# Kernel optimization log

Measured on AMD Instinct MI355X. Metric: run time of the kernel, lower is better.

Reference implementation:

```python
import jax, jax.numpy as jnp
import numpy as np

GRID_SIZE = 5
SPLINE_ORDER = 3
COEFF = GRID_SIZE + SPLINE_ORDER  # 8 spline coefficients per (out,in) pair
NUM_HEADS = 4
NUM_LAYERS = 4
DIM = 256
FF_DIM = 1024
VOCAB = 32000
EPS_EMB = 1e-12   # layernorm_eps from init
EPS_LN = 1e-5     # nn.LayerNorm default inside encoder layers


def make_grid(in_features):
    # uniform extended B-spline grid over [-1, 1], shape (in, grid_size + 2*order + 1)
    h = 2.0 / GRID_SIZE
    g = jnp.arange(-SPLINE_ORDER, GRID_SIZE + SPLINE_ORDER + 1, dtype=jnp.float32) * h - 1.0
    return jnp.broadcast_to(g, (in_features, g.shape[0]))


def b_splines(x, grid):
    # Cox-de Boor recursion. x: (..., in) -> (..., in, COEFF)
    xe = x[..., None]
    bases = ((xe >= grid[:, :-1]) & (xe < grid[:, 1:])).astype(x.dtype)
    for k in range(1, SPLINE_ORDER + 1):
        left = (xe - grid[:, : -(k + 1)]) / (grid[:, k:-1] - grid[:, : -(k + 1)])
        right = (grid[:, k + 1:] - xe) / (grid[:, k + 1:] - grid[:, 1:-k])
        bases = left * bases[..., :-1] + right * bases[..., 1:]
    return bases


def kan(x, base_w, spline_w):
    # efficient-kan KANLinear: silu base path + B-spline path
    grid = make_grid(x.shape[-1])
    base = jax.nn.silu(x) @ base_w.T
    spl = b_splines(x, grid)                      # (..., in, COEFF)
    return base + jnp.einsum('...ic,oic->...o', spl, spline_w)


def layer_norm(x, g=None, b=None, eps=EPS_LN):
    mu = jnp.mean(x, axis=-1, keepdims=True)
    var = jnp.mean((x - mu) ** 2, axis=-1, keepdims=True)
    y = (x - mu) * jax.lax.rsqrt(var + eps)
    return y * g + b if g is not None else y


def setup_inputs() -> dict:
    key = jax.random.key(0)
    ks = iter(jax.random.split(key, 64))

    def w(shape, s=0.02):
        return jax.random.normal(next(ks), shape, jnp.float32) * s

    inp = {
        'input_ids': jax.random.randint(next(ks), (2, 512), 0, VOCAB),
        'word_emb': w((VOCAB, DIM)),
        'tok_type_emb': w((2, DIM)),
        'pos_emb': w((512, DIM)),
        'emb_ln_g': jnp.ones((DIM,), jnp.float32),
        'emb_ln_b': jnp.zeros((DIM,), jnp.float32),
    }
    L = NUM_LAYERS
    for nm, (o, i) in [('q', (DIM, DIM)), ('k', (DIM, DIM)), ('v', (DIM, DIM)),
                       ('o', (DIM, DIM)), ('f1', (FF_DIM, DIM)), ('f2', (DIM, FF_DIM))]:
        inp[nm + '_base'] = w((L, o, i))
        inp[nm + '_spline'] = w((L, o, i, COEFF))
    inp['ln1_g'] = jnp.ones((L, DIM), jnp.float32)
    inp['ln1_b'] = jnp.zeros((L, DIM), jnp.float32)
    inp['ln2_g'] = jnp.ones((L, DIM), jnp.float32)
    inp['ln2_b'] = jnp.zeros((L, DIM), jnp.float32)
    inp['hk_base'] = w((DIM, DIM))
    inp['hk_spline'] = w((DIM, DIM, COEFF))
    inp['ho_base'] = w((VOCAB, DIM))
    inp['ho_spline'] = w((VOCAB, DIM, COEFF))
    return inp


def reference(input_ids, word_emb, tok_type_emb, pos_emb, emb_ln_g, emb_ln_b,
              q_base, q_spline, k_base, k_spline, v_base, v_spline,
              o_base, o_spline, f1_base, f1_spline, f2_base, f2_spline,
              ln1_g, ln1_b, ln2_g, ln2_b,
              hk_base, hk_spline, ho_base, ho_spline):
    B, S = input_ids.shape
    # Faithful to source: attention_mask defaults to ones_like(input_ids) and is
    # used to index BOTH token-type and positional embedding tables (row 1).
    x = word_emb[input_ids] + tok_type_emb[1] + pos_emb[1]
    x = layer_norm(x, emb_ln_g, emb_ln_b, eps=EPS_EMB)  # dropout = identity (deterministic)

    H, hd = NUM_HEADS, DIM // NUM_HEADS
    scale = hd ** -0.5
    for l in range(NUM_LAYERS):
        def split(t):
            return t.reshape(B, S, H, hd).transpose(0, 2, 1, 3)  # (B,H,S,hd)
        q = split(kan(x, q_base[l], q_spline[l]))
        k = split(kan(x, k_base[l], k_spline[l]))
        v = split(kan(x, v_base[l], v_spline[l]))
        attn = jax.nn.softmax(jnp.einsum('bhqd,bhkd->bhqk', q, k) * scale, axis=-1)
        ctx = jnp.einsum('bhqk,bhkd->bhqd', attn, v).transpose(0, 2, 1, 3).reshape(B, S, DIM)
        x = layer_norm(kan(ctx, o_base[l], o_spline[l]) + x, ln1_g[l], ln1_b[l])
        ff = kan(jax.nn.relu(kan(x, f1_base[l], f1_spline[l])), f2_base[l], f2_spline[l])
        x = layer_norm(ff + x, ln2_g[l], ln2_b[l])

    # GeneratorHead: KAN -> gelu -> layernorm(no affine) -> KAN to vocab
    h = jax.nn.gelu(kan(x, hk_base, hk_spline), approximate=False)
    h = layer_norm(h, eps=EPS_EMB)
    return kan(h, ho_base, ho_spline)  # (B, S, VOCAB)
```

## Files before the change

kernel.cpp:

```cpp
#include <hip/hip_runtime.h>
#include <math.h>

typedef unsigned short u16;
typedef unsigned int u32;
typedef __bf16 bf16x8 __attribute__((ext_vector_type(8)));
typedef float f32x4 __attribute__((ext_vector_type(4)));
typedef u16 us8 __attribute__((ext_vector_type(8)));

#define TOKENS 1024
#define DIM 256
#define SEQ 512


__device__ __forceinline__ u16 f2bf(float f) {
  u32 x = __float_as_uint(f);
  x += 0x7fffu + ((x >> 16) & 1u);
  return (u16)(x >> 16);
}

__device__ __forceinline__ void expand9(float x, u16* sil, us8* u) {
  float sig = 1.0f / (1.0f + expf(-x));
  *sil = f2bf(x * sig);
  float bs[11];
#pragma unroll
  for (int j = 0; j < 11; j++) {
    float gj  = (float)(j - 3) * 0.4f - 1.0f;
    float gj1 = (float)(j - 2) * 0.4f - 1.0f;
    bs[j] = (x >= gj && x < gj1) ? 1.0f : 0.0f;
  }
#pragma unroll
  for (int k = 1; k <= 3; k++) {
#pragma unroll
    for (int j = 0; j < 10; j++) {
      if (j + k < 11) {
        float gj   = (float)(j - 3) * 0.4f - 1.0f;
        float gj1  = (float)(j - 2) * 0.4f - 1.0f;
        float gjk  = (float)(j + k - 3) * 0.4f - 1.0f;
        float gjk1 = (float)(j + k - 2) * 0.4f - 1.0f;
        float linv = 1.0f / (gjk - gj);
        float rinv = 1.0f / (gjk1 - gj1);
        bs[j] = (x - gj) * linv * bs[j] + (gjk1 - x) * rinv * bs[j + 1];
      }
    }
  }
#pragma unroll
  for (int c = 0; c < 8; c++) (*u)[c] = f2bf(bs[c]);
}

__device__ __forceinline__ float block_sum_256(float v) {
  __shared__ float red[4];
  int t = threadIdx.x, lane = t & 63, wid = t >> 6;
#pragma unroll
  for (int o = 32; o > 0; o >>= 1) v += __shfl_down(v, o, 64);
  __syncthreads();
  if (lane == 0) red[wid] = v;
  __syncthreads();
  return red[0] + red[1] + red[2] + red[3];
}


__global__ void embed_ln_x(const int* __restrict__ ids, const float* __restrict__ wemb,
                           const float* __restrict__ tt, const float* __restrict__ pe,
                           const float* __restrict__ g, const float* __restrict__ bta,
                           float* __restrict__ xout, u16* __restrict__ Xe) {
  int row = blockIdx.x, t = threadIdx.x;
  int id = ids[row];
  float v = wemb[(size_t)id * DIM + t] + tt[DIM + t] + pe[DIM + t];
  float mu = block_sum_256(v) * (1.0f / 256.0f);
  float d = v - mu;
  float var = block_sum_256(d * d) * (1.0f / 256.0f);
  float y = d * rsqrtf(var + 1e-12f) * g[t] + bta[t];
  xout[(size_t)row * DIM + t] = y;
  size_t base = (size_t)row * 2304;
  u16 s; us8 u;
  expand9(y, &s, &u);
  Xe[base + t] = s;
  *(us8*)(Xe + base + 256 + (size_t)t * 8) = u;
}


__global__ void add_ln_x(const float* __restrict__ a, int nsum, int sstride,
                         const float* __restrict__ res,
                         const float* __restrict__ g, const float* __restrict__ bta,
                         float eps, int dogelu,
                         float* __restrict__ xout, u16* __restrict__ Xe) {
  int row = blockIdx.x, t = threadIdx.x;
  int idx = row * 256 + t;
  float v = 0.f;
  for (int s = 0; s < nsum; s++) v += a[(size_t)s * sstride + idx];
  if (dogelu) v = 0.5f * v * (1.0f + erff(v * 0.70710678118654752f));
  if (res) v += res[idx];
  float mu = block_sum_256(v) * (1.0f / 256.0f);
  float d = v - mu;
  float var = block_sum_256(d * d) * (1.0f / 256.0f);
  float y = d * rsqrtf(var + eps);
  if (g) y = y * g[t] + bta[t];
  xout[idx] = y;
  size_t base = (size_t)row * 2304;
  u16 s16; us8 u;
  expand9(y, &s16, &u);
  Xe[base + t] = s16;
  *(us8*)(Xe + base + 256 + (size_t)t * 8) = u;
}


#define LDA4(c, v) { int r_ = (c) * RPC + (t >> LGP); int g_ = t & (GPB - 1); \
    v = *(const uint4*)(A + (size_t)(m0 + r_) * K + k0n + g_ * 8); }
#define LDB4(c, va, vb) { int r_ = (c) * RPC + (t >> LGP); int g_ = t & (GPB - 1); \
    int kv_ = k0n + g_ * 8; \
    const float* p_ = (kv_ < infeat) ? (Wb + (size_t)(onb + r_) * infeat + kv_) \
                                     : (Ws + (size_t)(onb + r_) * infeat * 8 + (kv_ - infeat)); \
    va = *(const float4*)p_; vb = *(const float4*)(p_ + 4); }
#define STA4(c, v) { int r_ = (c) * RPC + (t >> LGP); int g_ = t & (GPB - 1); \
    *(uint4*)(&As[r_ * BK + ((g_ ^ (r_ & (GPB - 1))) << 3)]) = v; }
#define STB4(c, va, vb) { int r_ = (c) * RPC + (t >> LGP); int g_ = t & (GPB - 1); \
    bf16x8 h_; \
    h_[0] = (__bf16)va.x; h_[1] = (__bf16)va.y; h_[2] = (__bf16)va.z; h_[3] = (__bf16)va.w; \
    h_[4] = (__bf16)vb.x; h_[5] = (__bf16)vb.y; h_[6] = (__bf16)vb.z; h_[7] = (__bf16)vb.w; \
    *(bf16x8*)(&Bs[r_ * BK + ((g_ ^ (r_ & (GPB - 1))) << 3)]) = h_; }

template <int BM, int BN, int BK, int MINW, int EPI>
__global__ __launch_bounds__(256, MINW)
void gemm_kw(const u16* __restrict__ A,
             const float* __restrict__ b0, const float* __restrict__ s0,
             const float* __restrict__ b1, const float* __restrict__ s1,
             const float* __restrict__ b2, const float* __restrict__ s2,
             int nper, int N, int K, int infeat, int kchunk, float* __restrict__ C,
             u16* __restrict__ XeOut, int infOut) {
  constexpr int GPB = BK / 8;
  constexpr int LGP = (GPB == 8) ? 3 : 4;
  constexpr int RPC = 256 / GPB;
  static_assert(BM / RPC == 4 && BN / RPC == 4, "need exactly 4+4 chunks");
  constexpr int FM = BM / 32, FN = BN / 32;
  __shared__ u16 As[BM * BK];
  __shared__ u16 Bs[BN * BK];
  const int gx = gridDim.x;
  const int nwg = gx * gridDim.y;
  int g = blockIdx.y * gx + blockIdx.x;
  int lin = g;
  if ((nwg & 7) == 0) lin = (g & 7) * (nwg >> 3) + (g >> 3);
  const int m0 = (lin % gx) * BM;
  const int n0 = (lin / gx) * BN;
  const int z = blockIdx.z;
  const int kbeg = z * kchunk;
  const int kend = (kbeg + kchunk < K) ? kbeg + kchunk : K;
  const int t = threadIdx.x;
  const int lane = t & 63, wid = t >> 6;
  const int wm = (wid >> 1) * (BM / 2), wn = (wid & 1) * (BN / 2);
  const int proj = n0 / nper;
  const float* Wb = proj == 0 ? b0 : (proj == 1 ? b1 : b2);
  const float* Ws = proj == 0 ? s0 : (proj == 1 ? s1 : s2);
  const int onb = n0 - proj * nper;

  f32x4 acc[FM][FN];
#pragma unroll
  for (int i = 0; i < FM; i++)
#pragma unroll
    for (int j = 0; j < FN; j++) acc[i][j] = (f32x4){0.f, 0.f, 0.f, 0.f};

  const int frow = lane & 15;
  const int cgrp = lane >> 4;

  uint4 pa0, pa1, pa2, pa3;
  float4 pb0a, pb0b, pb1a, pb1b, pb2a, pb2b, pb3a, pb3b;
  int k0n = kbeg;
  LDA4(0, pa0); LDA4(1, pa1); LDA4(2, pa2); LDA4(3, pa3);
  LDB4(0, pb0a, pb0b); LDB4(1, pb1a, pb1b); LDB4(2, pb2a, pb2b); LDB4(3, pb3a, pb3b);

  for (int k0 = kbeg; k0 < kend; k0 += BK) {
    STA4(0, pa0); STA4(1, pa1); STA4(2, pa2); STA4(3, pa3);
    STB4(0, pb0a, pb0b); STB4(1, pb1a, pb1b); STB4(2, pb2a, pb2b); STB4(3, pb3a, pb3b);
    __syncthreads();
    if (k0 + BK < kend) {
      k0n = k0 + BK;
      LDA4(0, pa0); LDA4(1, pa1); LDA4(2, pa2); LDA4(3, pa3);
      LDB4(0, pb0a, pb0b); LDB4(1, pb1a, pb1b); LDB4(2, pb2a, pb2b); LDB4(3, pb3a, pb3b);
    }
#pragma unroll
    for (int kk = 0; kk < BK; kk += 32) {
      bf16x8 af[FM], bfr[FN];
#pragma unroll
      for (int i = 0; i < FM; i++) {
        int rr = wm + i * 16 + frow;
        int ch = (kk >> 3) + cgrp;
        af[i] = *reinterpret_cast<const bf16x8*>(&As[rr * BK + ((ch ^ (rr & (GPB - 1))) << 3)]);
      }
#pragma unroll
      for (int j = 0; j < FN; j++) {
        int rr = wn + j * 16 + frow;
        int ch = (kk >> 3) + cgrp;
        bfr[j] = *reinterpret_cast<const bf16x8*>(&Bs[rr * BK + ((ch ^ (rr & (GPB - 1))) << 3)]);
      }
#pragma unroll
      for (int i = 0; i < FM; i++)
#pragma unroll
        for (int j = 0; j < FN; j++)
          acc[i][j] = __builtin_amdgcn_mfma_f32_16x16x32_bf16(af[i], bfr[j], acc[i][j], 0, 0, 0);
    }
    __syncthreads();
  }

  const int crow = (lane >> 4) * 4;
  const int ccol = lane & 15;
  if constexpr (EPI == 0) {
    float* Cz = C + (size_t)z * TOKENS * N;
#pragma unroll
    for (int i = 0; i < FM; i++)
#pragma unroll
      for (int j = 0; j < FN; j++) {
        int row = m0 + wm + i * 16 + crow;
        int col = n0 + wn + j * 16 + ccol;
#pragma unroll
        for (int r = 0; r < 4; r++)
          Cz[(size_t)(row + r) * N + col] = acc[i][j][r];
      }
  } else {
    const int ldXe = infOut * 9;
#pragma unroll
    for (int i = 0; i < FM; i++)
#pragma unroll
      for (int j = 0; j < FN; j++) {
        int row0 = m0 + wm + i * 16 + crow;
        int col = n0 + wn + j * 16 + ccol;
#pragma unroll
        for (int r = 0; r < 4; r++) {
          float y = fmaxf(acc[i][j][r], 0.0f);
          u16 s; us8 u;
          expand9(y, &s, &u);
          size_t base = (size_t)(row0 + r) * ldXe;
          XeOut[base + col] = s;
          *(us8*)(XeOut + base + infOut + (size_t)col * 8) = u;
        }
      }
  }
}


__global__ void attn_fused(const float* __restrict__ qkv, u16* __restrict__ Xe) {
  const float* q1 = qkv + (size_t)TOKENS * 768;
  const float* q2 = qkv + (size_t)2 * TOKENS * 768;
  int bh = blockIdx.x, b = bh >> 2, h = bh & 3;
  int s0 = blockIdx.y * 16;
  int t = threadIdx.x;
  __shared__ float Qs[16][64];
  __shared__ float Ks[16][65];
  __shared__ float Ss[16][513];
  __shared__ float red[16][17];
  __shared__ float Vs[32][65];
#pragma unroll
  for (int c = 0; c < 4; c++) {
    int e = c * 256 + t, r = e >> 6, d = e & 63;
    size_t ix = (size_t)(b * SEQ + s0 + r) * 768 + h * 64 + d;
    Qs[r][d] = qkv[ix] + q1[ix] + q2[ix];
  }
  int r = t >> 4, cc = t & 15;
  for (int kc = 0; kc < SEQ; kc += 16) {
    __syncthreads();
#pragma unroll
    for (int c = 0; c < 4; c++) {
      int e = c * 256 + t, rr = e >> 6, d = e & 63;
      size_t ix = (size_t)(b * SEQ + kc + rr) * 768 + 256 + h * 64 + d;
      Ks[rr][d] = qkv[ix] + q1[ix] + q2[ix];
    }
    __syncthreads();
    float acc = 0.f;
#pragma unroll
    for (int d = 0; d < 64; d++) acc += Qs[r][d] * Ks[cc][d];
    Ss[r][kc + cc] = acc * 0.125f;
  }
  __syncthreads();
  float mx = -3.4e38f;
  for (int j = cc; j < SEQ; j += 16) mx = fmaxf(mx, Ss[r][j]);
  red[r][cc] = mx;
  __syncthreads();
  if (cc == 0) {
    float m = red[r][0];
#pragma unroll
    for (int j = 1; j < 16; j++) m = fmaxf(m, red[r][j]);
    red[r][16] = m;
  }
  __syncthreads();
  mx = red[r][16];
  float sm = 0.f;
  for (int j = cc; j < SEQ; j += 16) {
    float e = expf(Ss[r][j] - mx);
    Ss[r][j] = e;
    sm += e;
  }
  __syncthreads();
  red[r][cc] = sm;
  __syncthreads();
  if (cc == 0) {
    float s = 0.f;
#pragma unroll
    for (int j = 0; j < 16; j++) s += red[r][j];
    red[r][16] = s;
  }
  __syncthreads();
  float inv = 1.0f / red[r][16];
  for (int j = cc; j < SEQ; j += 16) Ss[r][j] *= inv;
  int dd = cc * 4;
  float a0 = 0.f, a1 = 0.f, a2 = 0.f, a3 = 0.f;
  for (int kc = 0; kc < SEQ; kc += 32) {
    __syncthreads();
#pragma unroll
    for (int c = 0; c < 8; c++) {
      int e = c * 256 + t, rr = e >> 6, d = e & 63;
      size_t ix = (size_t)(b * SEQ + kc + rr) * 768 + 512 + h * 64 + d;
      Vs[rr][d] = qkv[ix] + q1[ix] + q2[ix];
    }
    __syncthreads();
#pragma unroll
    for (int kk = 0; kk < 32; kk++) {
      float p = Ss[r][kc + kk];
      a0 += p * Vs[kk][dd + 0];
      a1 += p * Vs[kk][dd + 1];
      a2 += p * Vs[kk][dd + 2];
      a3 += p * Vs[kk][dd + 3];
    }
  }
  int row = b * SEQ + s0 + r;
  size_t base = (size_t)row * 2304;
  float av[4] = {a0, a1, a2, a3};
#pragma unroll
  for (int j = 0; j < 4; j++) {
    int col = h * 64 + dd + j;
    u16 s; us8 u;
    expand9(av[j], &s, &u);
    Xe[base + col] = s;
    *(us8*)(Xe + base + 256 + (size_t)col * 8) = u;
  }
}


extern "C" void kernel_launch(void* const* d_in, const int* in_sizes, int n_in,
                              void* d_out, int out_size, void* d_ws, size_t ws_size,
                              hipStream_t stream) {
  const int* ids = (const int*)d_in[0];
  const float* wemb = (const float*)d_in[1];
  const float* ttemb = (const float*)d_in[2];
  const float* pemb = (const float*)d_in[3];
  const float* elg = (const float*)d_in[4];
  const float* elb = (const float*)d_in[5];
  const float* qb = (const float*)d_in[6], *qs = (const float*)d_in[7];
  const float* kb = (const float*)d_in[8], *ks = (const float*)d_in[9];
  const float* vb = (const float*)d_in[10], *vs = (const float*)d_in[11];
  const float* ob = (const float*)d_in[12], *osp = (const float*)d_in[13];
  const float* f1b = (const float*)d_in[14], *f1s = (const float*)d_in[15];
  const float* f2b = (const float*)d_in[16], *f2s = (const float*)d_in[17];
  const float* l1g = (const float*)d_in[18], *l1b = (const float*)d_in[19];
  const float* l2g = (const float*)d_in[20], *l2b = (const float*)d_in[21];
  const float* hkb = (const float*)d_in[22], *hks = (const float*)d_in[23];
  const float* hob = (const float*)d_in[24], *hos = (const float*)d_in[25];
  float* out = (float*)d_out;

  char* w = (char*)d_ws;
  const size_t MB = 1 << 20;
  float* xbuf = (float*)(w);
  float* tmp  = (float*)(w + 1 * MB);
  float* qkv  = (float*)(w + 2 * MB);
  float* part = (float*)(w + 11 * MB);
  u16*   Xe2  = (u16*)  (w + 20 * MB);
  u16*   Xe   = (u16*)  (w + 38 * MB);

  embed_ln_x<<<TOKENS, 256, 0, stream>>>(ids, wemb, ttemb, pemb, elg, elb, xbuf, Xe);

  for (int l = 0; l < 4; l++) {
    const float* qbl = qb + (size_t)l * 65536, *qsl = qs + (size_t)l * 524288;
    const float* kbl = kb + (size_t)l * 65536, *ksl = ks + (size_t)l * 524288;
    const float* vbl = vb + (size_t)l * 65536, *vsl = vs + (size_t)l * 524288;
    const float* obl = ob + (size_t)l * 65536, *osl = osp + (size_t)l * 524288;
    const float* f1bl = f1b + (size_t)l * 262144, *f1sl = f1s + (size_t)l * 2097152;
    const float* f2bl = f2b + (size_t)l * 262144, *f2sl = f2s + (size_t)l * 2097152;

    gemm_kw<64, 64, 128, 2, 0><<<dim3(16, 12, 3), 256, 0, stream>>>(
        Xe, qbl, qsl, kbl, ksl, vbl, vsl, 256, 768, 2304, 256, 768, qkv, nullptr, 0);
    attn_fused<<<dim3(8, 32), 256, 0, stream>>>(qkv, Xe);
    gemm_kw<64, 64, 128, 2, 0><<<dim3(16, 4, 9), 256, 0, stream>>>(
        Xe, obl, osl, obl, osl, obl, osl, 256, 256, 2304, 256, 256, part, nullptr, 0);
    add_ln_x<<<TOKENS, 256, 0, stream>>>(part, 9, TOKENS * 256, xbuf,
                                         l1g + l * 256, l1b + l * 256, 1e-5f, 0, xbuf, Xe);
    gemm_kw<64, 64, 128, 2, 1><<<dim3(16, 16), 256, 0, stream>>>(
        Xe, f1bl, f1sl, f1bl, f1sl, f1bl, f1sl, 1024, 1024, 2304, 256, 2304,
        nullptr, Xe2, 1024);
    gemm_kw<64, 64, 128, 2, 0><<<dim3(16, 4, 8), 256, 0, stream>>>(
        Xe2, f2bl, f2sl, f2bl, f2sl, f2bl, f2sl, 256, 256, 9216, 1024, 1152,
        part, nullptr, 0);
    add_ln_x<<<TOKENS, 256, 0, stream>>>(part, 8, TOKENS * 256, xbuf,
                                         l2g + l * 256, l2b + l * 256, 1e-5f, 0, xbuf, Xe);
  }

  gemm_kw<64, 64, 128, 2, 0><<<dim3(16, 4, 9), 256, 0, stream>>>(
      Xe, hkb, hks, hkb, hks, hkb, hks, 256, 256, 2304, 256, 256, part, nullptr, 0);
  add_ln_x<<<TOKENS, 256, 0, stream>>>(part, 9, TOKENS * 256, nullptr, nullptr, nullptr,
                                       1e-12f, 1, tmp, Xe);
  gemm_kw<128, 128, 64, 1, 0><<<dim3(8, 250), 256, 0, stream>>>(
      Xe, hob, hos, hob, hos, hob, hos, 32000, 32000, 2304, 256, 2304, out, nullptr, 0);
}
```

Before: 902.0 us.

## Add dedicated 512-thread register-prefetched GEMM for vocab output head

```diff
diff --git a/kernel.cpp b/kernel.cpp
--- a/kernel.cpp
+++ b/kernel.cpp
@@ -236,6 +236,105 @@
 }
 
 
+__global__ __launch_bounds__(512, 1)
+void gemm_ho(const u16* __restrict__ A,
+             const float* __restrict__ Wb, const float* __restrict__ Ws,
+             int N, int K, int infeat, float* __restrict__ C) {
+  constexpr int BK = 64;
+  __shared__ u16 As[128 * BK];
+  __shared__ u16 Bs[128 * BK];
+  const int gx = gridDim.x;
+  const int nwg = gx * gridDim.y;
+  int g = blockIdx.y * gx + blockIdx.x;
+  int lin = g;
+  if ((nwg & 7) == 0) lin = (g & 7) * (nwg >> 3) + (g >> 3);
+  const int m0 = (lin % gx) * 128;
+  const int n0 = (lin / gx) * 128;
+  const int t = threadIdx.x;
+  const int lane = t & 63, wid = t >> 6;
+  const int wm = (wid >> 2) * 64, wn = (wid & 3) * 32;
+  const int rt = t >> 3, ct = t & 7;
+
+  f32x4 acc[4][2];
+#pragma unroll
+  for (int i = 0; i < 4; i++)
+#pragma unroll
+    for (int j = 0; j < 2; j++) acc[i][j] = (f32x4){0.f, 0.f, 0.f, 0.f};
+
+  const int frow = lane & 15;
+  const int cgrp = lane >> 4;
+
+  uint4 pa0, pa1;
+  float4 pb0a, pb0b, pb1a, pb1b;
+  int k0n = 0;
+
+#define LDH { \
+    pa0 = *(const uint4*)(A + (size_t)(m0 + rt) * K + k0n + ct * 8); \
+    pa1 = *(const uint4*)(A + (size_t)(m0 + 64 + rt) * K + k0n + ct * 8); \
+    int kv_ = k0n + ct * 8; \
+    const float* p0_ = (kv_ < infeat) ? (Wb + (size_t)(n0 + rt) * infeat + kv_) \
+                                      : (Ws + (size_t)(n0 + rt) * (size_t)infeat * 8 + (kv_ - infeat)); \
+    const float* p1_ = (kv_ < infeat) ? (Wb + (size_t)(n0 + 64 + rt) * infeat + kv_) \
+                                      : (Ws + (size_t)(n0 + 64 + rt) * (size_t)infeat * 8 + (kv_ - infeat)); \
+    pb0a = *(const float4*)p0_; pb0b = *(const float4*)(p0_ + 4); \
+    pb1a = *(const float4*)p1_; pb1b = *(const float4*)(p1_ + 4); }
+
+#define STH { \
+    *(uint4*)(&As[rt * BK + ((ct ^ (rt & 7)) << 3)]) = pa0; \
+    *(uint4*)(&As[(64 + rt) * BK + ((ct ^ (rt & 7)) << 3)]) = pa1; \
+    bf16x8 h0_, h1_; \
+    h0_[0]=(__bf16)pb0a.x; h0_[1]=(__bf16)pb0a.y; h0_[2]=(__bf16)pb0a.z; h0_[3]=(__bf16)pb0a.w; \
+    h0_[4]=(__bf16)pb0b.x; h0_[5]=(__bf16)pb0b.y; h0_[6]=(__bf16)pb0b.z; h0_[7]=(__bf16)pb0b.w; \
+    h1_[0]=(__bf16)pb1a.x; h1_[1]=(__bf16)pb1a.y; h1_[2]=(__bf16)pb1a.z; h1_[3]=(__bf16)pb1a.w; \
+    h1_[4]=(__bf16)pb1b.x; h1_[5]=(__bf16)pb1b.y; h1_[6]=(__bf16)pb1b.z; h1_[7]=(__bf16)pb1b.w; \
+    *(bf16x8*)(&Bs[rt * BK + ((ct ^ (rt & 7)) << 3)]) = h0_; \
+    *(bf16x8*)(&Bs[(64 + rt) * BK + ((ct ^ (rt & 7)) << 3)]) = h1_; }
+
+  LDH;
+  for (int k0 = 0; k0 < K; k0 += BK) {
+    STH;
+    __syncthreads();
+    if (k0 + BK < K) { k0n = k0 + BK; LDH; }
+#pragma unroll
+    for (int half = 0; half < 2; half++) {
+      const int ch = half * 4 + cgrp;
+      bf16x8 af[4], bfr[2];
+#pragma unroll
+      for (int i = 0; i < 4; i++) {
+        int rr = wm + i * 16 + frow;
+        af[i] = *reinterpret_cast<const bf16x8*>(&As[rr * BK + ((ch ^ (rr & 7)) << 3)]);
+      }
+#pragma unroll
+      for (int j = 0; j < 2; j++) {
+        int rr = wn + j * 16 + frow;
+        bfr[j] = *reinterpret_cast<const bf16x8*>(&Bs[rr * BK + ((ch ^ (rr & 7)) << 3)]);
+      }
+#pragma unroll
+      for (int i = 0; i < 4; i++)
+#pragma unroll
+        for (int j = 0; j < 2; j++)
+          acc[i][j] = __builtin_amdgcn_mfma_f32_16x16x32_bf16(af[i], bfr[j], acc[i][j], 0, 0, 0);
+    }
+    __syncthreads();
+  }
+#undef LDH
+#undef STH
+
+  const int crow = (lane >> 4) * 4;
+  const int ccol = lane & 15;
+#pragma unroll
+  for (int i = 0; i < 4; i++)
+#pragma unroll
+    for (int j = 0; j < 2; j++) {
+      int row = m0 + wm + i * 16 + crow;
+      int col = n0 + wn + j * 16 + ccol;
+#pragma unroll
+      for (int r = 0; r < 4; r++)
+        C[(size_t)(row + r) * N + col] = acc[i][j][r];
+    }
+}
+
+
 __global__ void attn_fused(const float* __restrict__ qkv, u16* __restrict__ Xe) {
   const float* q1 = qkv + (size_t)TOKENS * 768;
   const float* q2 = qkv + (size_t)2 * TOKENS * 768;
@@ -394,6 +493,5 @@
       Xe, hkb, hks, hkb, hks, hkb, hks, 256, 256, 2304, 256, 256, part, nullptr, 0);
   add_ln_x<<<TOKENS, 256, 0, stream>>>(part, 9, TOKENS * 256, nullptr, nullptr, nullptr,
                                        1e-12f, 1, tmp, Xe);
-  gemm_kw<128, 128, 64, 1, 0><<<dim3(8, 250), 256, 0, stream>>>(
-      Xe, hob, hos, hob, hos, hob, hos, 32000, 32000, 2304, 256, 2304, out, nullptr, 0);
-}
+  gemm_ho<<<dim3(8, 250), 512, 0, stream>>>(Xe, hob, hos, 32000, 2304, 256, out);
+}
```

Result: slower. 931.5 us (+3.3%).
